# Kernel tuning notes

Measured on AMD Instinct MI355X. Metric: run time of the kernel, lower is better.

## Reference

```python
import jax, jax.numpy as jnp
import numpy as np

B, S, D = 4, 2048, 1024  # batch, seq_len, isize; FFN hidden = isize, gate dim = 2*isize


def setup_inputs() -> dict:
    key = jax.random.key(0)
    ks = jax.random.split(key, 6)
    sc = lambda n: 1.0 / np.sqrt(n)
    return {
        "iQ": jax.random.normal(ks[0], (B, S, D), jnp.float32),
        "iV": jax.random.normal(ks[1], (B, S, D), jnp.float32),
        "W1": jax.random.normal(ks[2], (D, D), jnp.float32) * sc(D),
        "b1": jnp.zeros((D,), jnp.float32),
        "W2": jax.random.normal(ks[3], (D, D), jnp.float32) * sc(D),
        "b2": jnp.zeros((D,), jnp.float32),
        "Wg": jax.random.normal(ks[4], (2 * D, 2 * D), jnp.float32) * sc(2 * D),
        "bg": jnp.zeros((2 * D,), jnp.float32),
    }


def reference(iQ, iV, W1, b1, W2, b2, Wg, bg):
    seql = iV.shape[1]
    # AAN cumulative-average matrix: row i has 1/(i+1) in cols 0..i (lower triangular)
    inv = 1.0 / jnp.arange(1, seql + 1, dtype=iV.dtype)  # [S]
    attn = jnp.tril(jnp.broadcast_to(inv[:, None], (seql, seql)))  # [S, S]
    avg = jnp.einsum('st,btd->bsd', attn, iV)  # [B, S, D]
    # PositionwiseFF with norm_input=False, dropout=0: Linear -> ReLU -> Linear
    h = jax.nn.relu(avg @ W1 + b1)
    ffn = h @ W2 + b2  # [B, S, D]
    # sigmoid gate over concat(iQ, ffn)
    g = jax.nn.sigmoid(jnp.concatenate([iQ, ffn], axis=-1) @ Wg + bg)  # [B, S, 2D]
    d = ffn.shape[-1]
    igate = g[..., :d]
    fgate = g[..., d:]
    return igate * iQ + fgate * ffn
```

## Files before the change

kernel.cpp:

```cpp
#include <hip/hip_runtime.h>
#include <hip/hip_bf16.h>
#include <cstdint>

typedef unsigned short u16;
typedef unsigned int   u32;

typedef __attribute__((ext_vector_type(8))) short short8;
typedef __attribute__((ext_vector_type(4))) float f32x4;

__device__ __forceinline__ float b2f(u16 v) { return __uint_as_float(((u32)v) << 16); }
__device__ __forceinline__ u16 f2b(float f) {
    u32 u = __float_as_uint(f);
    u += 0x7FFFu + ((u >> 16) & 1u);
    return (u16)(u >> 16);
}

#define G2L16(gp, lp) __builtin_amdgcn_global_load_lds(                       \
    (const __attribute__((address_space(1))) void*)(gp),                      \
    (__attribute__((address_space(3))) void*)(lp), 16, 0, 0)

__device__ __forceinline__ void transpose_body(const float* __restrict__ in,
                                               u16* __restrict__ out,
                                               int R, int C, int lb, int tilesX,
                                               float (*tile)[33]) {
    const int bx = (lb % tilesX) * 32;
    const int by = (lb / tilesX) * 32;
    const int tx = threadIdx.x & 31, ty = threadIdx.x >> 5;
    #pragma unroll
    for (int i = 0; i < 32; i += 8)
        tile[ty + i][tx] = in[(size_t)(by + ty + i) * C + (bx + tx)];
    __syncthreads();
    #pragma unroll
    for (int i = 0; i < 32; i += 8)
        out[(size_t)(bx + ty + i) * R + (by + tx)] = f2b(tile[tx][ty + i]);
}

__global__ void prologue_kernel(const float* __restrict__ W1, u16* __restrict__ W1t,
                                const float* __restrict__ W2, u16* __restrict__ W2t,
                                const float* __restrict__ Wg, u16* __restrict__ Wgt,
                                const float* __restrict__ iQ, u16* __restrict__ iQb,
                                const float* __restrict__ iV, float* __restrict__ csum) {
    __shared__ float tile[32][33];
    const int bid = blockIdx.x;
    const int tid = threadIdx.x;
    if (bid < 1024) {
        transpose_body(W1, W1t, 1024, 1024, bid, 32, tile);
    } else if (bid < 2048) {
        transpose_body(W2, W2t, 1024, 1024, bid - 1024, 32, tile);
    } else if (bid < 6144) {
        transpose_body(Wg, Wgt, 2048, 2048, bid - 2048, 64, tile);
    } else if (bid < 14336) {
        const size_t i = ((size_t)(bid - 6144) * 256 + tid) * 4;
        const float4 v = *(const float4*)(iQ + i);
        ushort4 o;
        o.x = f2b(v.x); o.y = f2b(v.y); o.z = f2b(v.z); o.w = f2b(v.w);
        *(ushort4*)(iQb + i) = o;
    } else {
        const int idx = bid - 14336;
        const int b = idx >> 6, c = idx & 63;
        const int d = tid * 4;
        const float* src = iV + ((size_t)(b * 2048 + c * 32)) * 1024 + d;
        float4 s = {0.f, 0.f, 0.f, 0.f};
        #pragma unroll 8
        for (int i = 0; i < 32; ++i) {
            const float4 v = *(const float4*)(src + (size_t)i * 1024);
            s.x += v.x; s.y += v.y; s.z += v.z; s.w += v.w;
        }
        *(float4*)(csum + ((size_t)(b * 64 + c)) * 1024 + d) = s;
    }
}

__global__ void scan_kernel(const float* __restrict__ iV, const float* __restrict__ csum,
                            u16* __restrict__ avg) {
    const int c = blockIdx.x & 63, b = blockIdx.x >> 6;
    const int d = threadIdx.x * 4;
    const float* cs = csum + (size_t)b * 64 * 1024 + d;
    float4 a0 = {0,0,0,0}, a1 = {0,0,0,0}, a2 = {0,0,0,0}, a3 = {0,0,0,0};
    int cc = 0;
    for (; cc + 4 <= c; cc += 4) {
        const float4 v0 = *(const float4*)(cs + (size_t)(cc + 0) * 1024);
        const float4 v1 = *(const float4*)(cs + (size_t)(cc + 1) * 1024);
        const float4 v2 = *(const float4*)(cs + (size_t)(cc + 2) * 1024);
        const float4 v3 = *(const float4*)(cs + (size_t)(cc + 3) * 1024);
        a0.x += v0.x; a0.y += v0.y; a0.z += v0.z; a0.w += v0.w;
        a1.x += v1.x; a1.y += v1.y; a1.z += v1.z; a1.w += v1.w;
        a2.x += v2.x; a2.y += v2.y; a2.z += v2.z; a2.w += v2.w;
        a3.x += v3.x; a3.y += v3.y; a3.z += v3.z; a3.w += v3.w;
    }
    for (; cc < c; ++cc) {
        const float4 v = *(const float4*)(cs + (size_t)cc * 1024);
        a0.x += v.x; a0.y += v.y; a0.z += v.z; a0.w += v.w;
    }
    float4 acc;
    acc.x = (a0.x + a1.x) + (a2.x + a3.x);
    acc.y = (a0.y + a1.y) + (a2.y + a3.y);
    acc.z = (a0.z + a1.z) + (a2.z + a3.z);
    acc.w = (a0.w + a1.w) + (a2.w + a3.w);

    const size_t off = ((size_t)(b * 2048 + c * 32)) * 1024 + d;
    const float* src = iV + off;
    u16*         dst = avg + off;
    const int s0 = c * 32;
    #pragma unroll 4
    for (int i = 0; i < 32; ++i) {
        const float4 v = *(const float4*)(src + (size_t)i * 1024);
        acc.x += v.x; acc.y += v.y; acc.z += v.z; acc.w += v.w;
        const float inv = 1.0f / (float)(s0 + i + 1);
        ushort4 o;
        o.x = f2b(acc.x * inv); o.y = f2b(acc.y * inv);
        o.z = f2b(acc.z * inv); o.w = f2b(acc.w * inv);
        *(ushort4*)(dst + (size_t)i * 1024) = o;
    }
}

template <int EPI>
__global__ __launch_bounds__(256, 2)
void gemm_kernel(const u16* __restrict__ A, const u16* __restrict__ Bt,
                 const float* __restrict__ bias, u16* __restrict__ C,
                 int M, int N, int K) {
    __shared__ u16 As[128 * 64];
    __shared__ u16 Bs[128 * 64];

    const int tid  = threadIdx.x;
    const int m0   = blockIdx.x * 128;
    const int n0   = blockIdx.y * 128;
    const int wave = tid >> 6, lane = tid & 63;
    const int wm   = (wave & 1) << 6;
    const int wn   = (wave >> 1) << 6;
    const int quad = lane >> 4, l16 = lane & 15;

    f32x4 acc[4][4];
    #pragma unroll
    for (int i = 0; i < 4; ++i)
        #pragma unroll
        for (int j = 0; j < 4; ++j) acc[i][j] = (f32x4){0.f, 0.f, 0.f, 0.f};

    int oo[4], rr[4], qq[4];
    #pragma unroll
    for (int j = 0; j < 4; ++j) {
        oo[j] = tid * 16 + j * 4096;
        rr[j] = oo[j] >> 7;
        qq[j] = ((oo[j] >> 4) & 7) ^ (rr[j] & 7);
    }

    const int ktiles = K >> 6;
    for (int kt = 0; kt < ktiles; ++kt) {
        const int kb = kt << 6;
        #pragma unroll
        for (int j = 0; j < 4; ++j) {
            G2L16((const char*)A  + ((size_t)(m0 + rr[j]) * K + kb) * 2 + qq[j] * 16,
                  (char*)As + oo[j]);
            G2L16((const char*)Bt + ((size_t)(n0 + rr[j]) * K + kb) * 2 + qq[j] * 16,
                  (char*)Bs + oo[j]);
        }
        __syncthreads();

        #pragma unroll
        for (int h = 0; h < 2; ++h) {
            short8 af[4], bf[4];
            #pragma unroll
            for (int mi = 0; mi < 4; ++mi) {
                const int R = wm + mi * 16 + l16;
                af[mi] = *(const short8*)(As + R * 64 + ((((h << 2) | quad) ^ (R & 7)) << 3));
            }
            #pragma unroll
            for (int ni = 0; ni < 4; ++ni) {
                const int R = wn + ni * 16 + l16;
                bf[ni] = *(const short8*)(Bs + R * 64 + ((((h << 2) | quad) ^ (R & 7)) << 3));
            }
            #pragma unroll
            for (int mi = 0; mi < 4; ++mi)
                #pragma unroll
                for (int ni = 0; ni < 4; ++ni)
                    acc[mi][ni] = __builtin_amdgcn_mfma_f32_16x16x32_bf16(
                        af[mi], bf[ni], acc[mi][ni], 0, 0, 0);
        }
        __syncthreads();
    }

    #pragma unroll
    for (int ni = 0; ni < 4; ++ni) {
        const int col = n0 + wn + ni * 16 + l16;
        const float bv = bias[col];
        #pragma unroll
        for (int mi = 0; mi < 4; ++mi) {
            const int row0 = m0 + wm + mi * 16 + quad * 4;
            #pragma unroll
            for (int r = 0; r < 4; ++r) {
                float v = acc[mi][ni][r] + bv;
                if (EPI == 0) v = fmaxf(v, 0.f);
                C[(size_t)(row0 + r) * N + col] = f2b(v);
            }
        }
    }
}

__global__ __launch_bounds__(256, 2)
void gemm_gate_kernel(const u16* __restrict__ iQb, const u16* __restrict__ ffn,
                      const u16* __restrict__ Wgt, const float* __restrict__ bg,
                      const float* __restrict__ iQ, float* __restrict__ out,
                      int M, int D2 ) {
    __shared__ u16 As [128 * 32];
    __shared__ u16 Bs0[128 * 32];
    __shared__ u16 Bs1[128 * 32];

    const int tid  = threadIdx.x;
    const int m0   = blockIdx.x * 128;
    const int n0   = blockIdx.y * 128;
    const int wave = tid >> 6, lane = tid & 63;
    const int wm   = (wave & 1) << 6;
    const int wn   = (wave >> 1) << 6;
    const int quad = lane >> 4, l16 = lane & 15;
    const int D = D2 >> 1;

    f32x4 acc[2][4][4];
    #pragma unroll
    for (int p = 0; p < 2; ++p)
        #pragma unroll
        for (int i = 0; i < 4; ++i)
            #pragma unroll
            for (int j = 0; j < 4; ++j) acc[p][i][j] = (f32x4){0.f, 0.f, 0.f, 0.f};

    int oo[2], grow[2], gcol[2];
    #pragma unroll
    for (int j = 0; j < 2; ++j) {
        oo[j] = tid * 16 + j * 4096;
        const int rp = oo[j] >> 7;
        const int s  = (oo[j] >> 4) & 7;
        const int ch = s ^ (rp & 7);
        grow[j] = rp * 2 + (ch >> 2);
        gcol[j] = (ch & 3) * 16;
    }

    const int ktiles = D2 >> 5;
    for (int kt = 0; kt < ktiles; ++kt) {
        const int kb = kt << 5;
        const char* Ab = (const char*)((kb < D) ? (iQb + kb) : (ffn + (kb - D)));
        const char* B0 = (const char*)(Wgt + (size_t)n0 * D2 + kb);
        const char* B1 = (const char*)(Wgt + (size_t)(n0 + D) * D2 + kb);
        #pragma unroll
        for (int j = 0; j < 2; ++j) {
            G2L16(Ab + (size_t)(m0 + grow[j]) * D * 2 + gcol[j], (char*)As  + oo[j]);
            G2L16(B0 + (size_t)grow[j] * D2 * 2 + gcol[j],       (char*)Bs0 + oo[j]);
            G2L16(B1 + (size_t)grow[j] * D2 * 2 + gcol[j],       (char*)Bs1 + oo[j]);
        }
        __syncthreads();

        short8 af[4], bf0[4], bf1[4];
        #pragma unroll
        for (int mi = 0; mi < 4; ++mi) {
            const int R = wm + mi * 16 + l16;
            const int so = (R >> 1) * 64 +
                           (((((R & 1) << 2) | quad) ^ ((R >> 1) & 7)) << 3);
            af[mi] = *(const short8*)(As + so);
        }
        #pragma unroll
        for (int ni = 0; ni < 4; ++ni) {
            const int R = wn + ni * 16 + l16;
            const int so = (R >> 1) * 64 +
                           (((((R & 1) << 2) | quad) ^ ((R >> 1) & 7)) << 3);
            bf0[ni] = *(const short8*)(Bs0 + so);
            bf1[ni] = *(const short8*)(Bs1 + so);
        }
        #pragma unroll
        for (int mi = 0; mi < 4; ++mi)
            #pragma unroll
            for (int ni = 0; ni < 4; ++ni) {
                acc[0][mi][ni] = __builtin_amdgcn_mfma_f32_16x16x32_bf16(
                    af[mi], bf0[ni], acc[0][mi][ni], 0, 0, 0);
                acc[1][mi][ni] = __builtin_amdgcn_mfma_f32_16x16x32_bf16(
                    af[mi], bf1[ni], acc[1][mi][ni], 0, 0, 0);
            }
        __syncthreads();
    }

    #pragma unroll
    for (int ni = 0; ni < 4; ++ni) {
        const int col = n0 + wn + ni * 16 + l16;
        const float bgi = bg[col];
        const float bgf = bg[col + D];
        #pragma unroll
        for (int mi = 0; mi < 4; ++mi) {
            const int row0 = m0 + wm + mi * 16 + quad * 4;
            #pragma unroll
            for (int r = 0; r < 4; ++r) {
                const size_t idx = (size_t)(row0 + r) * D + col;
                const float gi = 1.0f / (1.0f + __expf(-(acc[0][mi][ni][r] + bgi)));
                const float gf = 1.0f / (1.0f + __expf(-(acc[1][mi][ni][r] + bgf)));
                out[idx] = gi * iQ[idx] + gf * b2f(ffn[idx]);
            }
        }
    }
}

extern "C" void kernel_launch(void* const* d_in, const int* in_sizes, int n_in,
                              void* d_out, int out_size, void* d_ws, size_t ws_size,
                              hipStream_t stream) {
    const int B = 4, S = 2048, D = 1024, D2 = 2048;
    const int M = B * S;

    const float* iQ = (const float*)d_in[0];
    const float* iV = (const float*)d_in[1];
    const float* W1 = (const float*)d_in[2];
    const float* b1 = (const float*)d_in[3];
    const float* W2 = (const float*)d_in[4];
    const float* b2 = (const float*)d_in[5];
    const float* Wg = (const float*)d_in[6];
    const float* bg = (const float*)d_in[7];
    float* out = (float*)d_out;

    u16*   regA = (u16*)d_ws;
    u16*   regB = regA + (size_t)M * D;
    u16*   iQb  = regB + (size_t)M * D;
    u16*   W1t  = iQb  + (size_t)M * D;
    u16*   W2t  = W1t  + (size_t)D * D;
    u16*   Wgt  = W2t  + (size_t)D * D;
    float* csum = (float*)(Wgt + (size_t)D2 * D2);

    u16* avg = regA;
    u16* ffn = regA;
    u16* h   = regB;

    prologue_kernel<<<14592, 256, 0, stream>>>(W1, W1t, W2, W2t, Wg, Wgt,
                                               iQ, iQb, iV, csum);
    scan_kernel<<<B * 64, 256, 0, stream>>>(iV, csum, avg);
    gemm_kernel<0><<<dim3(M / 128, D / 128), 256, 0, stream>>>(avg, W1t, b1, h, M, D, D);
    gemm_kernel<1><<<dim3(M / 128, D / 128), 256, 0, stream>>>(h, W2t, b2, ffn, M, D, D);
    gemm_gate_kernel<<<dim3(M / 128, D / 128), 256, 0, stream>>>(
        iQb, ffn, Wgt, bg, iQ, out, M, D2);
}
```

Baseline: 277.0 us.

## Fuse cumulative-average scan into prologue with per-block column-strip scan

Removes the separate scan kernel and csum buffer. Each of 128 prologue blocks now owns one batch and a 32-column strip: 8 thread groups each sum 256 rows, exchange partial sums through shared memory, then rescan their rows and write bf16 averages. This drops a kernel launch and the global round trip of the chunk sums, but only 128 blocks carry the scan, each thread loads one scalar with long serial dependent loops and reads iV twice, so the scan tail may run longer than before.

```diff
diff --git a/kernel.cpp b/kernel.cpp
--- a/kernel.cpp
+++ b/kernel.cpp
@@ -39,7 +39,7 @@
                                 const float* __restrict__ W2, u16* __restrict__ W2t,
                                 const float* __restrict__ Wg, u16* __restrict__ Wgt,
                                 const float* __restrict__ iQ, u16* __restrict__ iQb,
-                                const float* __restrict__ iV, float* __restrict__ csum) {
+                                const float* __restrict__ iV, u16* __restrict__ avg) {
     __shared__ float tile[32][33];
     const int bid = blockIdx.x;
     const int tid = threadIdx.x;
@@ -56,60 +56,28 @@
         o.x = f2b(v.x); o.y = f2b(v.y); o.z = f2b(v.z); o.w = f2b(v.w);
         *(ushort4*)(iQb + i) = o;
     } else {
-        const int idx = bid - 14336;
-        const int b = idx >> 6, c = idx & 63;
-        const int d = tid * 4;
-        const float* src = iV + ((size_t)(b * 2048 + c * 32)) * 1024 + d;
-        float4 s = {0.f, 0.f, 0.f, 0.f};
+        float (*psum)[32] = (float (*)[32])tile;
+        const int idx   = bid - 14336;
+        const int b     = idx >> 5;
+        const int strip = idx & 31;
+        const int d     = tid & 31;
+        const int g     = tid >> 5;
+        const int col   = strip * 32 + d;
+        const float* base = iV + ((size_t)(b * 2048 + g * 256)) * 1024 + col;
+        float s = 0.f;
         #pragma unroll 8
-        for (int i = 0; i < 32; ++i) {
-            const float4 v = *(const float4*)(src + (size_t)i * 1024);
-            s.x += v.x; s.y += v.y; s.z += v.z; s.w += v.w;
-        }
-        *(float4*)(csum + ((size_t)(b * 64 + c)) * 1024 + d) = s;
-    }
-}
-
-__global__ void scan_kernel(const float* __restrict__ iV, const float* __restrict__ csum,
-                            u16* __restrict__ avg) {
-    const int c = blockIdx.x & 63, b = blockIdx.x >> 6;
-    const int d = threadIdx.x * 4;
-    const float* cs = csum + (size_t)b * 64 * 1024 + d;
-    float4 a0 = {0,0,0,0}, a1 = {0,0,0,0}, a2 = {0,0,0,0}, a3 = {0,0,0,0};
-    int cc = 0;
-    for (; cc + 4 <= c; cc += 4) {
-        const float4 v0 = *(const float4*)(cs + (size_t)(cc + 0) * 1024);
-        const float4 v1 = *(const float4*)(cs + (size_t)(cc + 1) * 1024);
-        const float4 v2 = *(const float4*)(cs + (size_t)(cc + 2) * 1024);
-        const float4 v3 = *(const float4*)(cs + (size_t)(cc + 3) * 1024);
-        a0.x += v0.x; a0.y += v0.y; a0.z += v0.z; a0.w += v0.w;
-        a1.x += v1.x; a1.y += v1.y; a1.z += v1.z; a1.w += v1.w;
-        a2.x += v2.x; a2.y += v2.y; a2.z += v2.z; a2.w += v2.w;
-        a3.x += v3.x; a3.y += v3.y; a3.z += v3.z; a3.w += v3.w;
-    }
-    for (; cc < c; ++cc) {
-        const float4 v = *(const float4*)(cs + (size_t)cc * 1024);
-        a0.x += v.x; a0.y += v.y; a0.z += v.z; a0.w += v.w;
-    }
-    float4 acc;
-    acc.x = (a0.x + a1.x) + (a2.x + a3.x);
-    acc.y = (a0.y + a1.y) + (a2.y + a3.y);
-    acc.z = (a0.z + a1.z) + (a2.z + a3.z);
-    acc.w = (a0.w + a1.w) + (a2.w + a3.w);
-
-    const size_t off = ((size_t)(b * 2048 + c * 32)) * 1024 + d;
-    const float* src = iV + off;
-    u16*         dst = avg + off;
-    const int s0 = c * 32;
-    #pragma unroll 4
-    for (int i = 0; i < 32; ++i) {
-        const float4 v = *(const float4*)(src + (size_t)i * 1024);
-        acc.x += v.x; acc.y += v.y; acc.z += v.z; acc.w += v.w;
-        const float inv = 1.0f / (float)(s0 + i + 1);
-        ushort4 o;
-        o.x = f2b(acc.x * inv); o.y = f2b(acc.y * inv);
-        o.z = f2b(acc.z * inv); o.w = f2b(acc.w * inv);
-        *(ushort4*)(dst + (size_t)i * 1024) = o;
+        for (int i = 0; i < 256; ++i) s += base[(size_t)i * 1024];
+        psum[g][d] = s;
+        __syncthreads();
+        float acc = 0.f;
+        for (int gg = 0; gg < g; ++gg) acc += psum[gg][d];
+        u16* dst = avg + ((size_t)(b * 2048 + g * 256)) * 1024 + col;
+        const int s0 = g * 256;
+        #pragma unroll 8
+        for (int i = 0; i < 256; ++i) {
+            acc += base[(size_t)i * 1024];
+            dst[(size_t)i * 1024] = f2b(acc / (float)(s0 + i + 1));
+        }
     }
 }
 
@@ -309,21 +277,19 @@
     const float* bg = (const float*)d_in[7];
     float* out = (float*)d_out;
 
-    u16*   regA = (u16*)d_ws;
-    u16*   regB = regA + (size_t)M * D;
-    u16*   iQb  = regB + (size_t)M * D;
-    u16*   W1t  = iQb  + (size_t)M * D;
-    u16*   W2t  = W1t  + (size_t)D * D;
-    u16*   Wgt  = W2t  + (size_t)D * D;
-    float* csum = (float*)(Wgt + (size_t)D2 * D2);
+    u16* regA = (u16*)d_ws;
+    u16* regB = regA + (size_t)M * D;
+    u16* iQb  = regB + (size_t)M * D;
+    u16* W1t  = iQb  + (size_t)M * D;
+    u16* W2t  = W1t  + (size_t)D * D;
+    u16* Wgt  = W2t  + (size_t)D * D;
 
     u16* avg = regA;
     u16* ffn = regA;
     u16* h   = regB;
 
-    prologue_kernel<<<14592, 256, 0, stream>>>(W1, W1t, W2, W2t, Wg, Wgt,
-                                               iQ, iQb, iV, csum);
-    scan_kernel<<<B * 64, 256, 0, stream>>>(iV, csum, avg);
+    prologue_kernel<<<14464, 256, 0, stream>>>(W1, W1t, W2, W2t, Wg, Wgt,
+                                               iQ, iQb, iV, avg);
     gemm_kernel<0><<<dim3(M / 128, D / 128), 256, 0, stream>>>(avg, W1t, b1, h, M, D, D);
     gemm_kernel<1><<<dim3(M / 128, D / 128), 256, 0, stream>>>(h, W2t, b2, ffn, M, D, D);
     gemm_gate_kernel<<<dim3(M / 128, D / 128), 256, 0, stream>>>(
```

After: 311.7 us. +12.5%, slower.

## Fuse all stages into one persistent kernel with software grid barriers

Applied to the files above, without the earlier changes.

Replaces the five separate launches (prologue, scan, two FFN GEMMs, gate GEMM) with a single persistent 512-block kernel that runs each stage in turn, separated by atomic-counter grid barriers. The scan chunk size drops from 32 to 16 rows so that each of the 512 blocks owns one chunk. The aim is to remove launch gaps and tail effects between stages. In exchange, every stage is fixed to one block per output tile, the barriers add spin-wait cost, and correctness depends on all 512 blocks being co-resident.

```diff
diff --git a/kernel.cpp b/kernel.cpp
--- a/kernel.cpp
+++ b/kernel.cpp
@@ -18,6 +18,18 @@
 #define G2L16(gp, lp) __builtin_amdgcn_global_load_lds(                       \
     (const __attribute__((address_space(1))) void*)(gp),                      \
     (__attribute__((address_space(3))) void*)(lp), 16, 0, 0)
+
+#define GRID_BLOCKS 512u
+
+__device__ __forceinline__ void grid_barrier(u32* bar, u32 target) {
+    __syncthreads();
+    if (threadIdx.x == 0) {
+        __hip_atomic_fetch_add(bar, 1u, __ATOMIC_ACQ_REL, __HIP_MEMORY_SCOPE_AGENT);
+        while (__hip_atomic_load(bar, __ATOMIC_ACQUIRE, __HIP_MEMORY_SCOPE_AGENT) < target)
+            __builtin_amdgcn_s_sleep(2);
+    }
+    __syncthreads();
+}
 
 __device__ __forceinline__ void transpose_body(const float* __restrict__ in,
                                                u16* __restrict__ out,
@@ -35,95 +47,14 @@
         out[(size_t)(bx + ty + i) * R + (by + tx)] = f2b(tile[tx][ty + i]);
 }
 
-__global__ void prologue_kernel(const float* __restrict__ W1, u16* __restrict__ W1t,
-                                const float* __restrict__ W2, u16* __restrict__ W2t,
-                                const float* __restrict__ Wg, u16* __restrict__ Wgt,
-                                const float* __restrict__ iQ, u16* __restrict__ iQb,
-                                const float* __restrict__ iV, float* __restrict__ csum) {
-    __shared__ float tile[32][33];
-    const int bid = blockIdx.x;
-    const int tid = threadIdx.x;
-    if (bid < 1024) {
-        transpose_body(W1, W1t, 1024, 1024, bid, 32, tile);
-    } else if (bid < 2048) {
-        transpose_body(W2, W2t, 1024, 1024, bid - 1024, 32, tile);
-    } else if (bid < 6144) {
-        transpose_body(Wg, Wgt, 2048, 2048, bid - 2048, 64, tile);
-    } else if (bid < 14336) {
-        const size_t i = ((size_t)(bid - 6144) * 256 + tid) * 4;
-        const float4 v = *(const float4*)(iQ + i);
-        ushort4 o;
-        o.x = f2b(v.x); o.y = f2b(v.y); o.z = f2b(v.z); o.w = f2b(v.w);
-        *(ushort4*)(iQb + i) = o;
-    } else {
-        const int idx = bid - 14336;
-        const int b = idx >> 6, c = idx & 63;
-        const int d = tid * 4;
-        const float* src = iV + ((size_t)(b * 2048 + c * 32)) * 1024 + d;
-        float4 s = {0.f, 0.f, 0.f, 0.f};
-        #pragma unroll 8
-        for (int i = 0; i < 32; ++i) {
-            const float4 v = *(const float4*)(src + (size_t)i * 1024);
-            s.x += v.x; s.y += v.y; s.z += v.z; s.w += v.w;
-        }
-        *(float4*)(csum + ((size_t)(b * 64 + c)) * 1024 + d) = s;
-    }
-}
-
-__global__ void scan_kernel(const float* __restrict__ iV, const float* __restrict__ csum,
-                            u16* __restrict__ avg) {
-    const int c = blockIdx.x & 63, b = blockIdx.x >> 6;
-    const int d = threadIdx.x * 4;
-    const float* cs = csum + (size_t)b * 64 * 1024 + d;
-    float4 a0 = {0,0,0,0}, a1 = {0,0,0,0}, a2 = {0,0,0,0}, a3 = {0,0,0,0};
-    int cc = 0;
-    for (; cc + 4 <= c; cc += 4) {
-        const float4 v0 = *(const float4*)(cs + (size_t)(cc + 0) * 1024);
-        const float4 v1 = *(const float4*)(cs + (size_t)(cc + 1) * 1024);
-        const float4 v2 = *(const float4*)(cs + (size_t)(cc + 2) * 1024);
-        const float4 v3 = *(const float4*)(cs + (size_t)(cc + 3) * 1024);
-        a0.x += v0.x; a0.y += v0.y; a0.z += v0.z; a0.w += v0.w;
-        a1.x += v1.x; a1.y += v1.y; a1.z += v1.z; a1.w += v1.w;
-        a2.x += v2.x; a2.y += v2.y; a2.z += v2.z; a2.w += v2.w;
-        a3.x += v3.x; a3.y += v3.y; a3.z += v3.z; a3.w += v3.w;
-    }
-    for (; cc < c; ++cc) {
-        const float4 v = *(const float4*)(cs + (size_t)cc * 1024);
-        a0.x += v.x; a0.y += v.y; a0.z += v.z; a0.w += v.w;
-    }
-    float4 acc;
-    acc.x = (a0.x + a1.x) + (a2.x + a3.x);
-    acc.y = (a0.y + a1.y) + (a2.y + a3.y);
-    acc.z = (a0.z + a1.z) + (a2.z + a3.z);
-    acc.w = (a0.w + a1.w) + (a2.w + a3.w);
-
-    const size_t off = ((size_t)(b * 2048 + c * 32)) * 1024 + d;
-    const float* src = iV + off;
-    u16*         dst = avg + off;
-    const int s0 = c * 32;
-    #pragma unroll 4
-    for (int i = 0; i < 32; ++i) {
-        const float4 v = *(const float4*)(src + (size_t)i * 1024);
-        acc.x += v.x; acc.y += v.y; acc.z += v.z; acc.w += v.w;
-        const float inv = 1.0f / (float)(s0 + i + 1);
-        ushort4 o;
-        o.x = f2b(acc.x * inv); o.y = f2b(acc.y * inv);
-        o.z = f2b(acc.z * inv); o.w = f2b(acc.w * inv);
-        *(ushort4*)(dst + (size_t)i * 1024) = o;
-    }
-}
-
 template <int EPI>
-__global__ __launch_bounds__(256, 2)
-void gemm_kernel(const u16* __restrict__ A, const u16* __restrict__ Bt,
-                 const float* __restrict__ bias, u16* __restrict__ C,
-                 int M, int N, int K) {
-    __shared__ u16 As[128 * 64];
-    __shared__ u16 Bs[128 * 64];
+__device__ void gemm_body(const u16* __restrict__ A, const u16* __restrict__ Bt,
+                          const float* __restrict__ bias, u16* __restrict__ C,
+                          int N, int K, int m0, int n0, char* smemraw) {
+    u16* As = (u16*)smemraw;
+    u16* Bs = (u16*)(smemraw + 16384);
 
     const int tid  = threadIdx.x;
-    const int m0   = blockIdx.x * 128;
-    const int n0   = blockIdx.y * 128;
     const int wave = tid >> 6, lane = tid & 63;
     const int wm   = (wave & 1) << 6;
     const int wn   = (wave >> 1) << 6;
@@ -195,23 +126,20 @@
     }
 }
 
-__global__ __launch_bounds__(256, 2)
-void gemm_gate_kernel(const u16* __restrict__ iQb, const u16* __restrict__ ffn,
-                      const u16* __restrict__ Wgt, const float* __restrict__ bg,
-                      const float* __restrict__ iQ, float* __restrict__ out,
-                      int M, int D2 ) {
-    __shared__ u16 As [128 * 32];
-    __shared__ u16 Bs0[128 * 32];
-    __shared__ u16 Bs1[128 * 32];
+__device__ void gate_body(const u16* __restrict__ iQb, const u16* __restrict__ ffn,
+                          const u16* __restrict__ Wgt, const float* __restrict__ bg,
+                          const float* __restrict__ iQ, float* __restrict__ out,
+                          int m0, int n0, char* smemraw) {
+    u16* As  = (u16*)smemraw;
+    u16* Bs0 = (u16*)(smemraw + 8192);
+    u16* Bs1 = (u16*)(smemraw + 16384);
 
     const int tid  = threadIdx.x;
-    const int m0   = blockIdx.x * 128;
-    const int n0   = blockIdx.y * 128;
     const int wave = tid >> 6, lane = tid & 63;
     const int wm   = (wave & 1) << 6;
     const int wn   = (wave >> 1) << 6;
     const int quad = lane >> 4, l16 = lane & 15;
-    const int D = D2 >> 1;
+    const int D = 1024, D2 = 2048;
 
     f32x4 acc[2][4][4];
     #pragma unroll
@@ -293,11 +221,107 @@
     }
 }
 
+__global__ __launch_bounds__(256, 2)
+void fused_kernel(const float* __restrict__ iQ, const float* __restrict__ iV,
+                  const float* __restrict__ W1, const float* __restrict__ b1,
+                  const float* __restrict__ W2, const float* __restrict__ b2,
+                  const float* __restrict__ Wg, const float* __restrict__ bg,
+                  float* __restrict__ out,
+                  u16* __restrict__ regA,
+                  u16* __restrict__ h,
+                  u16* __restrict__ iQb,
+                  u16* __restrict__ W1t, u16* __restrict__ W2t,
+                  u16* __restrict__ Wgt, float* __restrict__ csum,
+                  u32* __restrict__ bar) {
+    __shared__ __align__(16) char smem[32768];
+    const int bid = blockIdx.x;
+    const int tid = threadIdx.x;
+
+    {
+        float (*tile)[33] = (float (*)[33])smem;
+        for (int job = bid; job < 6144; job += GRID_BLOCKS) {
+            if (job < 1024)      transpose_body(W1, W1t, 1024, 1024, job, 32, tile);
+            else if (job < 2048) transpose_body(W2, W2t, 1024, 1024, job - 1024, 32, tile);
+            else                 transpose_body(Wg, Wgt, 2048, 2048, job - 2048, 64, tile);
+            __syncthreads();
+        }
+        const int b = bid >> 7, c = bid & 127;
+        const float* src = iV + ((size_t)(b * 2048 + c * 16)) * 1024 + tid * 4;
+        float4 s = {0.f, 0.f, 0.f, 0.f};
+        #pragma unroll
+        for (int i = 0; i < 16; ++i) {
+            const float4 v = *(const float4*)(src + (size_t)i * 1024);
+            s.x += v.x; s.y += v.y; s.z += v.z; s.w += v.w;
+        }
+        *(float4*)(csum + ((size_t)(b * 128 + c)) * 1024 + tid * 4) = s;
+    }
+    grid_barrier(bar, 1 * GRID_BLOCKS);
+
+    {
+        const int b = bid >> 7, c = bid & 127;
+        const int d = tid * 4;
+        const float* cs = csum + (size_t)b * 128 * 1024 + d;
+        float4 a0 = {0,0,0,0}, a1 = {0,0,0,0}, a2 = {0,0,0,0}, a3 = {0,0,0,0};
+        int cc = 0;
+        for (; cc + 4 <= c; cc += 4) {
+            const float4 v0 = *(const float4*)(cs + (size_t)(cc + 0) * 1024);
+            const float4 v1 = *(const float4*)(cs + (size_t)(cc + 1) * 1024);
+            const float4 v2 = *(const float4*)(cs + (size_t)(cc + 2) * 1024);
+            const float4 v3 = *(const float4*)(cs + (size_t)(cc + 3) * 1024);
+            a0.x += v0.x; a0.y += v0.y; a0.z += v0.z; a0.w += v0.w;
+            a1.x += v1.x; a1.y += v1.y; a1.z += v1.z; a1.w += v1.w;
+            a2.x += v2.x; a2.y += v2.y; a2.z += v2.z; a2.w += v2.w;
+            a3.x += v3.x; a3.y += v3.y; a3.z += v3.z; a3.w += v3.w;
+        }
+        for (; cc < c; ++cc) {
+            const float4 v = *(const float4*)(cs + (size_t)cc * 1024);
+            a0.x += v.x; a0.y += v.y; a0.z += v.z; a0.w += v.w;
+        }
+        float4 acc;
+        acc.x = (a0.x + a1.x) + (a2.x + a3.x);
+        acc.y = (a0.y + a1.y) + (a2.y + a3.y);
+        acc.z = (a0.z + a1.z) + (a2.z + a3.z);
+        acc.w = (a0.w + a1.w) + (a2.w + a3.w);
+
+        const size_t off = ((size_t)(b * 2048 + c * 16)) * 1024 + d;
+        const float* src = iV + off;
+        u16*         dst = regA + off;
+        const int s0 = c * 16;
+        #pragma unroll
+        for (int i = 0; i < 16; ++i) {
+            const float4 v = *(const float4*)(src + (size_t)i * 1024);
+            acc.x += v.x; acc.y += v.y; acc.z += v.z; acc.w += v.w;
+            const float inv = 1.0f / (float)(s0 + i + 1);
+            ushort4 o;
+            o.x = f2b(acc.x * inv); o.y = f2b(acc.y * inv);
+            o.z = f2b(acc.z * inv); o.w = f2b(acc.w * inv);
+            *(ushort4*)(dst + (size_t)i * 1024) = o;
+        }
+        const float4* iq4 = (const float4*)iQ;
+        ushort4* qb4 = (ushort4*)iQb;
+        for (int j = bid * 256 + tid; j < (8192 * 1024 / 4); j += GRID_BLOCKS * 256) {
+            const float4 v = iq4[j];
+            ushort4 o;
+            o.x = f2b(v.x); o.y = f2b(v.y); o.z = f2b(v.z); o.w = f2b(v.w);
+            qb4[j] = o;
+        }
+    }
+    grid_barrier(bar, 2 * GRID_BLOCKS);
+
+    gemm_body<0>(regA, W1t, b1, h, 1024, 1024, (bid >> 3) * 128, (bid & 7) * 128, smem);
+    grid_barrier(bar, 3 * GRID_BLOCKS);
+
+    gemm_body<1>(h, W2t, b2, regA, 1024, 1024, (bid >> 3) * 128, (bid & 7) * 128, smem);
+    grid_barrier(bar, 4 * GRID_BLOCKS);
+
+    gate_body(iQb, regA, Wgt, bg, iQ, out, (bid >> 3) * 128, (bid & 7) * 128, smem);
+}
+
 extern "C" void kernel_launch(void* const* d_in, const int* in_sizes, int n_in,
                               void* d_out, int out_size, void* d_ws, size_t ws_size,
                               hipStream_t stream) {
-    const int B = 4, S = 2048, D = 1024, D2 = 2048;
-    const int M = B * S;
+    const int D = 1024, D2 = 2048;
+    const int M = 8192;
 
     const float* iQ = (const float*)d_in[0];
     const float* iV = (const float*)d_in[1];
@@ -310,22 +334,16 @@
     float* out = (float*)d_out;
 
     u16*   regA = (u16*)d_ws;
-    u16*   regB = regA + (size_t)M * D;
-    u16*   iQb  = regB + (size_t)M * D;
+    u16*   h    = regA + (size_t)M * D;
+    u16*   iQb  = h    + (size_t)M * D;
     u16*   W1t  = iQb  + (size_t)M * D;
     u16*   W2t  = W1t  + (size_t)D * D;
     u16*   Wgt  = W2t  + (size_t)D * D;
     float* csum = (float*)(Wgt + (size_t)D2 * D2);
-
-    u16* avg = regA;
-    u16* ffn = regA;
-    u16* h   = regB;
-
-    prologue_kernel<<<14592, 256, 0, stream>>>(W1, W1t, W2, W2t, Wg, Wgt,
-                                               iQ, iQb, iV, csum);
-    scan_kernel<<<B * 64, 256, 0, stream>>>(iV, csum, avg);
-    gemm_kernel<0><<<dim3(M / 128, D / 128), 256, 0, stream>>>(avg, W1t, b1, h, M, D, D);
-    gemm_kernel<1><<<dim3(M / 128, D / 128), 256, 0, stream>>>(h, W2t, b2, ffn, M, D, D);
-    gemm_gate_kernel<<<dim3(M / 128, D / 128), 256, 0, stream>>>(
-        iQb, ffn, Wgt, bg, iQ, out, M, D2);
-}
+    u32*   bar  = (u32*)(csum + (size_t)4 * 128 * 1024);
+
+    hipMemsetAsync(bar, 0, 64, stream);
+    fused_kernel<<<GRID_BLOCKS, 256, 0, stream>>>(
+        iQ, iV, W1, b1, W2, b2, Wg, bg, out,
+        regA, h, iQb, W1t, W2t, Wgt, csum, bar);
+}
```

After: 580.7 us. 2.1x slower.
